# Performance work log

Measured on AMD Instinct MI355X. Metric: run time of the kernel, lower is better.

## Reference

```python
import jax, jax.numpy as jnp
import numpy as np

N_NODES = 50000
N_EDGES = 1250000
D_IN = 64
D_HID = 64
D_OUT = 16
N_GRAPHS = 128


def setup_inputs() -> dict:
    key = jax.random.key(0)
    ks = jax.random.split(key, 16)
    glorot = lambda k, shape: jax.random.normal(k, shape, jnp.float32) * (2.0 / (shape[0] + shape[1])) ** 0.5
    inp = {
        "x": jax.random.normal(ks[0], (N_NODES, D_IN), jnp.float32),
        "edge_index": jax.random.randint(ks[1], (2, N_EDGES), 0, N_NODES, jnp.int32),
        "adj": jnp.zeros((1,), jnp.float32),
        "batch": jnp.sort(jax.random.randint(ks[2], (N_NODES,), 0, N_GRAPHS, jnp.int32)),
        # GraphConv layer 1: lin_rel (with bias) on aggregated msgs, lin_root (no bias) on x
        "W_rel1": glorot(ks[3], (D_IN, D_HID)),
        "b_rel1": jnp.zeros((D_HID,), jnp.float32),
        "W_root1": glorot(ks[4], (D_IN, D_HID)),
        "W_rel2": glorot(ks[5], (D_HID, D_HID)),
        "b_rel2": jnp.zeros((D_HID,), jnp.float32),
        "W_root2": glorot(ks[6], (D_HID, D_HID)),
        "W_rel3": glorot(ks[7], (D_HID, D_HID)),
        "b_rel3": jnp.zeros((D_HID,), jnp.float32),
        "W_root3": glorot(ks[8], (D_HID, D_HID)),
        "W_lin": glorot(ks[9], (D_HID, D_OUT)),
        "b_lin": jnp.zeros((D_OUT,), jnp.float32),
    }
    return inp


def graph_conv(x, src, dst, W_rel, b_rel, W_root):
    # PyG GraphConv (aggr='add'): out[i] = (sum_{j->i} x[j]) @ W_rel + b_rel + x[i] @ W_root
    agg = jax.ops.segment_sum(x[src], dst, num_segments=N_NODES)  # [N, d]
    return agg @ W_rel + b_rel + x @ W_root


def reference(x, edge_index, adj, batch,
              W_rel1, b_rel1, W_root1,
              W_rel2, b_rel2, W_root2,
              W_rel3, b_rel3, W_root3,
              W_lin, b_lin):
    src, dst = edge_index[0], edge_index[1]
    h = jax.nn.relu(graph_conv(x, src, dst, W_rel1, b_rel1, W_root1))
    h = jax.nn.relu(graph_conv(h, src, dst, W_rel2, b_rel2, W_root2))
    h = graph_conv(h, src, dst, W_rel3, b_rel3, W_root3)
    # global_mean_pool over batch ids
    sums = jax.ops.segment_sum(h, batch, num_segments=N_GRAPHS)  # [G, d]
    counts = jax.ops.segment_sum(jnp.ones((h.shape[0],), h.dtype), batch, num_segments=N_GRAPHS)
    pooled = sums / jnp.maximum(counts, 1.0)[:, None]
    return pooled @ W_lin + b_lin  # [G, D_OUT]
```

## Files before the change

### kernel.cpp

```cpp
#include <hip/hip_runtime.h>

#define D 64
#define N_GRAPHS 128
#define D_OUT 16
#define BCAP 16384
#define TILE 4096

typedef unsigned short u16;
typedef unsigned int u32;
typedef unsigned char u8;
typedef __attribute__((ext_vector_type(8))) short bf16x8;
typedef __attribute__((ext_vector_type(4))) float f32x4;

__device__ inline u16 f2bf(float f) {
  u32 u = __float_as_uint(f);
  return (u16)((u + 0x7fffu + ((u >> 16) & 1u)) >> 16);
}
__device__ inline float bf2f(u16 b) { return __uint_as_float((u32)b << 16); }

__global__ __launch_bounds__(256) void cvt_bf16_kernel(
    const float* __restrict__ in, u16* __restrict__ out, int n4,
    int* __restrict__ cursors, int nbuck,
    const float* __restrict__ Wrel1, const float* __restrict__ Wroot1,
    const float* __restrict__ Wrel2, const float* __restrict__ Wroot2,
    const float* __restrict__ Wrel3, const float* __restrict__ Wroot3,
    const float* __restrict__ Wlin, const float* __restrict__ brel3,
    const float* __restrict__ blin,
    float* __restrict__ M1, float* __restrict__ M2, float* __restrict__ cvec,
    u16* __restrict__ WbT1r, u16* __restrict__ WbT1o,
    u16* __restrict__ WbT2r, u16* __restrict__ WbT2o) {
  int t = threadIdx.x;
  if (blockIdx.x == 0) {
    if (t < nbuck) cursors[t] = t * BCAP;
    if (t >= 240) {
      int o = t - 240;
      float c = blin[o];
#pragma unroll
      for (int j = 0; j < D; j++) c = fmaf(brel3[j], Wlin[j * D_OUT + o], c);
      cvec[o] = c;
    }
  } else if (blockIdx.x <= 8) {
    int idx = (blockIdx.x - 1) * 256 + t;
    const float* W = (idx < 1024) ? Wrel3 : Wroot3;
    float* M = (idx < 1024) ? M1 : M2;
    int id = idx & 1023;
    int k = id >> 4, o = id & 15;
    float acc = 0.0f;
#pragma unroll
    for (int j = 0; j < D; j++) acc = fmaf(W[k * D + j], Wlin[j * D_OUT + o], acc);
    M[id] = acc;
  } else if (blockIdx.x <= 16) {
    int tid = (blockIdx.x - 9) * 256 + t;
    int mat = tid >> 9;
    int r = tid & 511;
    int o = r >> 3;
    int k0 = (r & 7) * 8;
    const float* Wsrc = (mat == 0) ? Wrel1 : (mat == 1) ? Wroot1
                       : (mat == 2) ? Wrel2 : Wroot2;
    u16* Wdst = (mat == 0) ? WbT1r : (mat == 1) ? WbT1o
               : (mat == 2) ? WbT2r : WbT2o;
    u16 tmp[8];
#pragma unroll
    for (int j = 0; j < 8; j++) tmp[j] = f2bf(Wsrc[(k0 + j) * D + o]);
    uint4 pw;
    pw.x = (u32)tmp[0] | ((u32)tmp[1] << 16);
    pw.y = (u32)tmp[2] | ((u32)tmp[3] << 16);
    pw.z = (u32)tmp[4] | ((u32)tmp[5] << 16);
    pw.w = (u32)tmp[6] | ((u32)tmp[7] << 16);
    *(uint4*)&Wdst[o * D + k0] = pw;
  }
  int i = blockIdx.x * 256 + t;
  if (i >= n4) return;
  float4 v = ((const float4*)in)[i];
  ushort4 o4;
  o4.x = f2bf(v.x); o4.y = f2bf(v.y); o4.z = f2bf(v.z); o4.w = f2bf(v.w);
  ((ushort4*)out)[i] = o4;
}

__global__ __launch_bounds__(256) void bin_kernel(
    const int* __restrict__ src, const int* __restrict__ dst,
    int* __restrict__ cursors, u32* __restrict__ binned,
    int n_edges, int nbuck) {
  __shared__ u32 ent[TILE];
  __shared__ u8 ebk[TILE];
  __shared__ int hist[256];
  __shared__ int startb[256];
  __shared__ int cur[256];
  __shared__ int gbase[256];
  int t = threadIdx.x;
  hist[t] = 0;
  __syncthreads();

  int base = blockIdx.x * TILE;
  int cnt = n_edges - base;
  if (cnt > TILE) cnt = TILE;

  int mys[16], myd[16];
#pragma unroll
  for (int j = 0; j < 16; j++) {
    int i = base + t + j * 256;
    if (t + j * 256 < cnt) {
      mys[j] = src[i];
      myd[j] = dst[i];
      atomicAdd(&hist[myd[j] >> 8], 1);
    } else {
      myd[j] = -1;
    }
  }
  __syncthreads();
  int myc = hist[t];
  for (int off = 1; off < 256; off <<= 1) {
    int tmp = (t >= off) ? hist[t - off] : 0;
    __syncthreads();
    hist[t] += tmp;
    __syncthreads();
  }
  int excl = hist[t] - myc;
  startb[t] = excl;
  cur[t] = excl;
  __syncthreads();

#pragma unroll
  for (int j = 0; j < 16; j++) {
    if (myd[j] >= 0) {
      int b = myd[j] >> 8;
      int p = atomicAdd(&cur[b], 1);
      ent[p] = ((u32)myd[j] << 16) | (u32)mys[j];
      ebk[p] = (u8)b;
    }
  }
  __syncthreads();

  if (t < nbuck && myc > 0) gbase[t] = atomicAdd(&cursors[t], myc);
  __syncthreads();

#pragma unroll
  for (int j = 0; j < 16; j++) {
    int p = t + j * 256;
    if (p < cnt) {
      int b = ebk[p];
      int gpos = gbase[b] + (p - startb[b]);
      if (gpos < (b + 1) * BCAP) binned[gpos] = ent[p];
    }
  }
}

__global__ __launch_bounds__(256) void csr_kernel(
    const u32* __restrict__ binned, const int* __restrict__ cursors,
    u16* __restrict__ csr_src, int* __restrict__ offsets,
    int n_nodes, int nbuck) {
  __shared__ int deg[256];
  __shared__ int cur[256];
  __shared__ int red[256];
  __shared__ u16 lcsr[BCAP];
  int b = blockIdx.x, t = threadIdx.x;
  int cnt = cursors[b] - b * BCAP;
  if (cnt < 0) cnt = 0;
  if (cnt > BCAP) cnt = BCAP;

  int c = 0;
  if (t < b) {
    c = cursors[t] - t * BCAP;
    if (c < 0) c = 0;
    if (c > BCAP) c = BCAP;
  }
  red[t] = c;
  __syncthreads();
  for (int off = 128; off > 0; off >>= 1) {
    if (t < off) red[t] += red[t + off];
    __syncthreads();
  }
  int ebase = red[0];

  int nodeBase = b << 8;
  int nn = n_nodes - nodeBase;
  if (nn > 256) nn = 256;

  deg[t] = 0;
  __syncthreads();
  const u32* be = binned + (size_t)b * BCAP;
  for (int i = t; i < cnt; i += 256)
    atomicAdd(&deg[(be[i] >> 16) - nodeBase], 1);
  __syncthreads();
  int myd = deg[t];
  for (int off = 1; off < 256; off <<= 1) {
    int tmp = (t >= off) ? deg[t - off] : 0;
    __syncthreads();
    deg[t] += tmp;
    __syncthreads();
  }
  int loff = deg[t] - myd;
  cur[t] = loff;
  if (t < nn) offsets[nodeBase + t] = ebase + loff;
  if (b == nbuck - 1 && t == 0) offsets[n_nodes] = ebase + cnt;
  __syncthreads();

  for (int i = t; i < cnt; i += 256) {
    u32 e = be[i];
    int ln = (e >> 16) - nodeBase;
    int p = atomicAdd(&cur[ln], 1);
    lcsr[p] = (u16)(e & 0xffffu);
  }
  __syncthreads();
  for (int i = t; i < cnt; i += 256) csr_src[ebase + i] = lcsr[i];
}

#define ACC8(a, r)                                                       \
  a[0] += __uint_as_float(r.x << 16); a[1] += __uint_as_float(r.x & 0xffff0000u); \
  a[2] += __uint_as_float(r.y << 16); a[3] += __uint_as_float(r.y & 0xffff0000u); \
  a[4] += __uint_as_float(r.z << 16); a[5] += __uint_as_float(r.z & 0xffff0000u); \
  a[6] += __uint_as_float(r.w << 16); a[7] += __uint_as_float(r.w & 0xffff0000u);

__global__ __launch_bounds__(256) void fused_layer_kernel(
    const u16* __restrict__ h, const int* __restrict__ offsets,
    const u16* __restrict__ csr_src,
    const u16* __restrict__ WbTrel, const u16* __restrict__ WbTroot,
    const float* __restrict__ brel,
    u16* __restrict__ h_out, int n_nodes, int do_relu) {
  __shared__ __align__(16) u16 ldsA[32 * 72];
  __shared__ __align__(16) u16 ldsX[32 * 72];
  int w = threadIdx.x >> 6;
  int lane = threadIdx.x & 63;
  int sub = lane >> 3;
  int fo = (lane & 7) * 8;
  int blockBase = blockIdx.x * 32;
  int nid = blockBase + w * 8 + sub;
  bool valid = nid < n_nodes;
  int node = valid ? nid : 0;
  int start = offsets[node];
  int end = offsets[node + 1];
  if (!valid) end = start;
  int lrow = (w * 8 + sub) * 72;

  uint4 xr = make_uint4(0, 0, 0, 0);
  if (valid) xr = *(const uint4*)(h + ((size_t)node << 6) + fo);
  *(uint4*)&ldsX[lrow + fo] = xr;

  float a0[8] = {0, 0, 0, 0, 0, 0, 0, 0};
  float a1[8] = {0, 0, 0, 0, 0, 0, 0, 0};
  int i = start;
  for (; i + 3 < end; i += 4) {
    int s0 = csr_src[i], s1 = csr_src[i + 1], s2 = csr_src[i + 2], s3 = csr_src[i + 3];
    uint4 r0 = *(const uint4*)(h + ((size_t)s0 << 6) + fo);
    uint4 r1 = *(const uint4*)(h + ((size_t)s1 << 6) + fo);
    uint4 r2 = *(const uint4*)(h + ((size_t)s2 << 6) + fo);
    uint4 r3 = *(const uint4*)(h + ((size_t)s3 << 6) + fo);
    ACC8(a0, r0) ACC8(a1, r1) ACC8(a0, r2) ACC8(a1, r3)
  }
  for (; i < end; i++) {
    int s0 = csr_src[i];
    uint4 r0 = *(const uint4*)(h + ((size_t)s0 << 6) + fo);
    ACC8(a0, r0)
  }
#pragma unroll
  for (int k = 0; k < 8; k++) a0[k] += a1[k];

  uint4 pa;
  pa.x = (u32)f2bf(a0[0]) | ((u32)f2bf(a0[1]) << 16);
  pa.y = (u32)f2bf(a0[2]) | ((u32)f2bf(a0[3]) << 16);
  pa.z = (u32)f2bf(a0[4]) | ((u32)f2bf(a0[5]) << 16);
  pa.w = (u32)f2bf(a0[6]) | ((u32)f2bf(a0[7]) << 16);
  *(uint4*)&ldsA[lrow + fo] = pa;
  __syncthreads();

  int mt = w & 1;
  int ntb = (w >> 1) * 2;
  int lr = lane & 15, lk = lane >> 4;
  int arow = (mt * 16 + lr) * 72;
  bf16x8 af0 = *(const bf16x8*)&ldsA[arow + lk * 8];
  bf16x8 af1 = *(const bf16x8*)&ldsA[arow + 32 + lk * 8];
  bf16x8 xf0 = *(const bf16x8*)&ldsX[arow + lk * 8];
  bf16x8 xf1 = *(const bf16x8*)&ldsX[arow + 32 + lk * 8];
#pragma unroll
  for (int tt = 0; tt < 2; tt++) {
    int nt = ntb + tt;
    int wrow = (nt * 16 + lr) * D + lk * 8;
    bf16x8 br0 = *(const bf16x8*)(WbTrel + wrow);
    bf16x8 br1 = *(const bf16x8*)(WbTrel + wrow + 32);
    bf16x8 bo0 = *(const bf16x8*)(WbTroot + wrow);
    bf16x8 bo1 = *(const bf16x8*)(WbTroot + wrow + 32);
    f32x4 acc = {0.0f, 0.0f, 0.0f, 0.0f};
    acc = __builtin_amdgcn_mfma_f32_16x16x32_bf16(af0, br0, acc, 0, 0, 0);
    acc = __builtin_amdgcn_mfma_f32_16x16x32_bf16(af1, br1, acc, 0, 0, 0);
    acc = __builtin_amdgcn_mfma_f32_16x16x32_bf16(xf0, bo0, acc, 0, 0, 0);
    acc = __builtin_amdgcn_mfma_f32_16x16x32_bf16(xf1, bo1, acc, 0, 0, 0);
    float bias = brel[nt * 16 + lr];
#pragma unroll
    for (int r = 0; r < 4; r++) {
      int onode = blockBase + mt * 16 + lk * 4 + r;
      if (onode < n_nodes) {
        float v = acc[r] + bias;
        if (do_relu) v = fmaxf(v, 0.0f);
        h_out[((size_t)onode << 6) + nt * 16 + lr] = f2bf(v);
      }
    }
  }
}

__global__ __launch_bounds__(256) void gather_kernel(
    const u16* __restrict__ h, const int* __restrict__ offsets,
    const u16* __restrict__ csr_src, float* __restrict__ agg, int n_nodes) {
  int wave = blockIdx.x * 4 + (threadIdx.x >> 6);
  int lane = threadIdx.x & 63;
  int sub = lane >> 3;
  int fo = (lane & 7) * 8;
  int nid = wave * 8 + sub;
  bool valid = nid < n_nodes;
  int node = valid ? nid : 0;
  int start = offsets[node];
  int end = offsets[node + 1];
  if (!valid) end = start;

  float a0[8] = {0, 0, 0, 0, 0, 0, 0, 0};
  float a1[8] = {0, 0, 0, 0, 0, 0, 0, 0};
  int i = start;
  for (; i + 3 < end; i += 4) {
    int s0 = csr_src[i], s1 = csr_src[i + 1], s2 = csr_src[i + 2], s3 = csr_src[i + 3];
    uint4 r0 = *(const uint4*)(h + ((size_t)s0 << 6) + fo);
    uint4 r1 = *(const uint4*)(h + ((size_t)s1 << 6) + fo);
    uint4 r2 = *(const uint4*)(h + ((size_t)s2 << 6) + fo);
    uint4 r3 = *(const uint4*)(h + ((size_t)s3 << 6) + fo);
    ACC8(a0, r0) ACC8(a1, r1) ACC8(a0, r2) ACC8(a1, r3)
  }
  for (; i < end; i++) {
    int s0 = csr_src[i];
    uint4 r0 = *(const uint4*)(h + ((size_t)s0 << 6) + fo);
    ACC8(a0, r0)
  }
#pragma unroll
  for (int k = 0; k < 8; k++) a0[k] += a1[k];
  if (valid) {
    float* ap = agg + ((size_t)node << 6) + fo;
    *(float4*)(ap)     = make_float4(a0[0], a0[1], a0[2], a0[3]);
    *(float4*)(ap + 4) = make_float4(a0[4], a0[5], a0[6], a0[7]);
  }
}

__global__ __launch_bounds__(256) void pool_mean2_kernel(
    const float* __restrict__ aggA, const u16* __restrict__ hH,
    const int* __restrict__ batch, float* __restrict__ pooledA,
    float* __restrict__ pooledH, float* __restrict__ pooledCnt, int n_nodes) {
  __shared__ int seg[2];
  __shared__ float redA[256], redH[256];
  int g = blockIdx.x;
  if (threadIdx.x < 2) {
    int target = g + (int)threadIdx.x;
    int lo = 0, hi = n_nodes;
    while (lo < hi) {
      int mid = (lo + hi) >> 1;
      if (batch[mid] < target) lo = mid + 1; else hi = mid;
    }
    seg[threadIdx.x] = lo;
  }
  __syncthreads();
  int start = seg[0], end = seg[1];
  int f = threadIdx.x & 63, sub = threadIdx.x >> 6;
  float aA = 0.0f, aH = 0.0f;
  for (int n = start + sub; n < end; n += 4) {
    aA += aggA[((size_t)n << 6) + f];
    aH += bf2f(hH[((size_t)n << 6) + f]);
  }
  redA[threadIdx.x] = aA;
  redH[threadIdx.x] = aH;
  __syncthreads();
  if (sub == 0) {
    float vA = redA[f] + redA[64 + f] + redA[128 + f] + redA[192 + f];
    float vH = redH[f] + redH[64 + f] + redH[128 + f] + redH[192 + f];
    float cnt = (float)(end - start);
    float inv = 1.0f / fmaxf(cnt, 1.0f);
    pooledA[g * D + f] = vA * inv;
    pooledH[g * D + f] = vH * inv;
    if (f == 0) pooledCnt[g] = cnt;
  }
}

__global__ __launch_bounds__(256) void final2_kernel(
    const float* __restrict__ pooledA, const float* __restrict__ pooledH,
    const float* __restrict__ M1, const float* __restrict__ M2,
    const float* __restrict__ cvec, const float* __restrict__ blin,
    const float* __restrict__ pooledCnt, float* __restrict__ out) {
  int idx = blockIdx.x * 256 + threadIdx.x;
  if (idx >= N_GRAPHS * D_OUT) return;
  int g = idx >> 4;
  int o = idx & 15;
  float acc = (pooledCnt[g] > 0.0f) ? cvec[o] : blin[o];
#pragma unroll
  for (int k = 0; k < D; k++) {
    acc = fmaf(pooledA[g * D + k], M1[k * D_OUT + o], acc);
    acc = fmaf(pooledH[g * D + k], M2[k * D_OUT + o], acc);
  }
  out[idx] = acc;
}

extern "C" void kernel_launch(void* const* d_in, const int* in_sizes, int n_in,
                              void* d_out, int out_size, void* d_ws, size_t ws_size,
                              hipStream_t stream) {
  const float* x     = (const float*)d_in[0];
  const int*   ei    = (const int*)d_in[1];
  const int*   batch = (const int*)d_in[3];
  const float* Wrel1 = (const float*)d_in[4];
  const float* brel1 = (const float*)d_in[5];
  const float* Wroot1= (const float*)d_in[6];
  const float* Wrel2 = (const float*)d_in[7];
  const float* brel2 = (const float*)d_in[8];
  const float* Wroot2= (const float*)d_in[9];
  const float* Wrel3 = (const float*)d_in[10];
  const float* brel3 = (const float*)d_in[11];
  const float* Wroot3= (const float*)d_in[12];
  const float* Wlin  = (const float*)d_in[13];
  const float* blin  = (const float*)d_in[14];
  float* out = (float*)d_out;

  const int n_edges = in_sizes[1] / 2;
  const int n_nodes = in_sizes[0] / D;
  const int* src = ei;
  const int* dst = ei + n_edges;
  const int nbuck = (n_nodes + 255) >> 8;

  char* p = (char*)d_ws;
  size_t binned_bytes = (size_t)nbuck * BCAP * sizeof(u32);
  size_t agg_bytes = (size_t)n_nodes * D * sizeof(float);
  u32* binned  = (u32*)p;
  float* agg   = (float*)p;
  p += (binned_bytes > agg_bytes ? binned_bytes : agg_bytes);
  float* pooledA = (float*)p; p += (size_t)N_GRAPHS * D * sizeof(float);
  float* pooledH = (float*)p; p += (size_t)N_GRAPHS * D * sizeof(float);
  float* pooledCnt = (float*)p; p += (size_t)N_GRAPHS * sizeof(float);
  float* M1     = (float*)p; p += (size_t)D * D_OUT * sizeof(float);
  float* M2     = (float*)p; p += (size_t)D * D_OUT * sizeof(float);
  float* cvec   = (float*)p; p += 16 * sizeof(float);
  int* cursors  = (int*)p;   p += 256 * sizeof(int);
  int* offsets  = (int*)p;   p += (size_t)(n_nodes + 4) * sizeof(int);
  u16* hX       = (u16*)p;   p += (size_t)n_nodes * D * sizeof(u16);
  u16* h1       = (u16*)p;   p += (size_t)n_nodes * D * sizeof(u16);
  u16* h2       = (u16*)p;   p += (size_t)n_nodes * D * sizeof(u16);
  u16* csr_src  = (u16*)p;   p += (size_t)n_edges * sizeof(u16);
  u16* WbT1r    = (u16*)p;   p += (size_t)D * D * sizeof(u16);
  u16* WbT1o    = (u16*)p;   p += (size_t)D * D * sizeof(u16);
  u16* WbT2r    = (u16*)p;   p += (size_t)D * D * sizeof(u16);
  u16* WbT2o    = (u16*)p;   p += (size_t)D * D * sizeof(u16);

  const int bin_blocks = (n_edges + TILE - 1) / TILE;
  const int fused_blocks = (n_nodes + 31) / 32;
  const int gath_blocks = (n_nodes + 31) / 32;
  const int cvt_n4 = n_nodes * D / 4;

  cvt_bf16_kernel<<<(cvt_n4 + 255) / 256, 256, 0, stream>>>(
      x, hX, cvt_n4, cursors, nbuck, Wrel1, Wroot1, Wrel2, Wroot2,
      Wrel3, Wroot3, Wlin, brel3, blin, M1, M2, cvec,
      WbT1r, WbT1o, WbT2r, WbT2o);
  bin_kernel<<<bin_blocks, 256, 0, stream>>>(src, dst, cursors, binned, n_edges, nbuck);
  csr_kernel<<<nbuck, 256, 0, stream>>>(binned, cursors, csr_src, offsets, n_nodes, nbuck);

  fused_layer_kernel<<<fused_blocks, 256, 0, stream>>>(
      hX, offsets, csr_src, WbT1r, WbT1o, brel1, h1, n_nodes, 1);
  fused_layer_kernel<<<fused_blocks, 256, 0, stream>>>(
      h1, offsets, csr_src, WbT2r, WbT2o, brel2, h2, n_nodes, 1);

  gather_kernel<<<gath_blocks, 256, 0, stream>>>(h2, offsets, csr_src, agg, n_nodes);

  pool_mean2_kernel<<<N_GRAPHS, 256, 0, stream>>>(agg, h2, batch, pooledA, pooledH, pooledCnt, n_nodes);
  final2_kernel<<<(N_GRAPHS * D_OUT + 255) / 256, 256, 0, stream>>>(
      pooledA, pooledH, M1, M2, cvec, blin, pooledCnt, out);
}
```

Baseline: 256.2 us.

## Degree-sort nodes per wave, pack bf16 accumulation, fuse pool and final kernels

Each 32-node block now ranks its nodes by in-degree in a shared-memory prologue and assigns them to 8-lane groups in sorted order, so each wave holds nodes of similar degree and wastes fewer idle lanes in the gather loop. The accumulators become two-float vectors to allow packed adds. The pooling kernel and the final projection kernel are merged into one launch, which drops the intermediate pooled buffers. The prologue costs two extra barriers and an O(32) rank loop per block.

```diff
diff --git a/kernel.cpp b/kernel.cpp
--- a/kernel.cpp
+++ b/kernel.cpp
@@ -11,12 +11,16 @@
 typedef unsigned char u8;
 typedef __attribute__((ext_vector_type(8))) short bf16x8;
 typedef __attribute__((ext_vector_type(4))) float f32x4;
+typedef __attribute__((ext_vector_type(2))) float f32x2;
 
 __device__ inline u16 f2bf(float f) {
   u32 u = __float_as_uint(f);
   return (u16)((u + 0x7fffu + ((u >> 16) & 1u)) >> 16);
 }
 __device__ inline float bf2f(u16 b) { return __uint_as_float((u32)b << 16); }
+__device__ inline f32x2 bfpair(u32 v) {
+  return (f32x2){__uint_as_float(v << 16), __uint_as_float(v & 0xffff0000u)};
+}
 
 __global__ __launch_bounds__(256) void cvt_bf16_kernel(
     const float* __restrict__ in, u16* __restrict__ out, int n4,
@@ -205,11 +209,29 @@
   for (int i = t; i < cnt; i += 256) csr_src[ebase + i] = lcsr[i];
 }
 
-#define ACC8(a, r)                                                       \
-  a[0] += __uint_as_float(r.x << 16); a[1] += __uint_as_float(r.x & 0xffff0000u); \
-  a[2] += __uint_as_float(r.y << 16); a[3] += __uint_as_float(r.y & 0xffff0000u); \
-  a[4] += __uint_as_float(r.z << 16); a[5] += __uint_as_float(r.z & 0xffff0000u); \
-  a[6] += __uint_as_float(r.w << 16); a[7] += __uint_as_float(r.w & 0xffff0000u);
+#define ACC8(a, r) \
+  a[0] += bfpair(r.x); a[1] += bfpair(r.y); a[2] += bfpair(r.z); a[3] += bfpair(r.w);
+
+#define BALANCE_PROLOGUE(soff, permAr, blockBase, n_nodes, offsets)     \
+  {                                                                     \
+    int t_ = threadIdx.x;                                               \
+    if (t_ < 33) {                                                      \
+      int idx = blockBase + t_;                                         \
+      if (idx > n_nodes) idx = n_nodes;                                 \
+      soff[t_] = offsets[idx];                                          \
+    }                                                                   \
+    __syncthreads();                                                    \
+    if (t_ < 32) {                                                      \
+      int d_ = (blockBase + t_ < n_nodes) ? soff[t_ + 1] - soff[t_] : -1; \
+      int r_ = 0;                                                       \
+      for (int j_ = 0; j_ < 32; j_++) {                                 \
+        int dj_ = (blockBase + j_ < n_nodes) ? soff[j_ + 1] - soff[j_] : -1; \
+        if (dj_ > d_ || (dj_ == d_ && j_ < t_)) r_++;                   \
+      }                                                                 \
+      permAr[r_] = (u8)t_;                                              \
+    }                                                                   \
+    __syncthreads();                                                    \
+  }
 
 __global__ __launch_bounds__(256) void fused_layer_kernel(
     const u16* __restrict__ h, const int* __restrict__ offsets,
@@ -219,25 +241,30 @@
     u16* __restrict__ h_out, int n_nodes, int do_relu) {
   __shared__ __align__(16) u16 ldsA[32 * 72];
   __shared__ __align__(16) u16 ldsX[32 * 72];
+  __shared__ int soff[33];
+  __shared__ u8 permAr[32];
   int w = threadIdx.x >> 6;
   int lane = threadIdx.x & 63;
   int sub = lane >> 3;
   int fo = (lane & 7) * 8;
   int blockBase = blockIdx.x * 32;
-  int nid = blockBase + w * 8 + sub;
-  bool valid = nid < n_nodes;
-  int node = valid ? nid : 0;
-  int start = offsets[node];
-  int end = offsets[node + 1];
+
+  BALANCE_PROLOGUE(soff, permAr, blockBase, n_nodes, offsets)
+
+  int ln = permAr[w * 8 + sub];
+  int node = blockBase + ln;
+  bool valid = node < n_nodes;
+  int start = soff[ln];
+  int end = soff[ln + 1];
   if (!valid) end = start;
-  int lrow = (w * 8 + sub) * 72;
+  int lrow = ln * 72;
 
   uint4 xr = make_uint4(0, 0, 0, 0);
   if (valid) xr = *(const uint4*)(h + ((size_t)node << 6) + fo);
   *(uint4*)&ldsX[lrow + fo] = xr;
 
-  float a0[8] = {0, 0, 0, 0, 0, 0, 0, 0};
-  float a1[8] = {0, 0, 0, 0, 0, 0, 0, 0};
+  f32x2 a0[4] = {{0,0},{0,0},{0,0},{0,0}};
+  f32x2 a1[4] = {{0,0},{0,0},{0,0},{0,0}};
   int i = start;
   for (; i + 3 < end; i += 4) {
     int s0 = csr_src[i], s1 = csr_src[i + 1], s2 = csr_src[i + 2], s3 = csr_src[i + 3];
@@ -253,13 +280,13 @@
     ACC8(a0, r0)
   }
 #pragma unroll
-  for (int k = 0; k < 8; k++) a0[k] += a1[k];
+  for (int k = 0; k < 4; k++) a0[k] += a1[k];
 
   uint4 pa;
-  pa.x = (u32)f2bf(a0[0]) | ((u32)f2bf(a0[1]) << 16);
-  pa.y = (u32)f2bf(a0[2]) | ((u32)f2bf(a0[3]) << 16);
-  pa.z = (u32)f2bf(a0[4]) | ((u32)f2bf(a0[5]) << 16);
-  pa.w = (u32)f2bf(a0[6]) | ((u32)f2bf(a0[7]) << 16);
+  pa.x = (u32)f2bf(a0[0].x) | ((u32)f2bf(a0[0].y) << 16);
+  pa.y = (u32)f2bf(a0[1].x) | ((u32)f2bf(a0[1].y) << 16);
+  pa.z = (u32)f2bf(a0[2].x) | ((u32)f2bf(a0[2].y) << 16);
+  pa.w = (u32)f2bf(a0[3].x) | ((u32)f2bf(a0[3].y) << 16);
   *(uint4*)&ldsA[lrow + fo] = pa;
   __syncthreads();
 
@@ -300,19 +327,25 @@
 __global__ __launch_bounds__(256) void gather_kernel(
     const u16* __restrict__ h, const int* __restrict__ offsets,
     const u16* __restrict__ csr_src, float* __restrict__ agg, int n_nodes) {
-  int wave = blockIdx.x * 4 + (threadIdx.x >> 6);
+  __shared__ int soff[33];
+  __shared__ u8 permAr[32];
+  int w = threadIdx.x >> 6;
   int lane = threadIdx.x & 63;
   int sub = lane >> 3;
   int fo = (lane & 7) * 8;
-  int nid = wave * 8 + sub;
-  bool valid = nid < n_nodes;
-  int node = valid ? nid : 0;
-  int start = offsets[node];
-  int end = offsets[node + 1];
+  int blockBase = blockIdx.x * 32;
+
+  BALANCE_PROLOGUE(soff, permAr, blockBase, n_nodes, offsets)
+
+  int ln = permAr[w * 8 + sub];
+  int node = blockBase + ln;
+  bool valid = node < n_nodes;
+  int start = soff[ln];
+  int end = soff[ln + 1];
   if (!valid) end = start;
 
-  float a0[8] = {0, 0, 0, 0, 0, 0, 0, 0};
-  float a1[8] = {0, 0, 0, 0, 0, 0, 0, 0};
+  f32x2 a0[4] = {{0,0},{0,0},{0,0},{0,0}};
+  f32x2 a1[4] = {{0,0},{0,0},{0,0},{0,0}};
   int i = start;
   for (; i + 3 < end; i += 4) {
     int s0 = csr_src[i], s1 = csr_src[i + 1], s2 = csr_src[i + 2], s3 = csr_src[i + 3];
@@ -328,68 +361,63 @@
     ACC8(a0, r0)
   }
 #pragma unroll
-  for (int k = 0; k < 8; k++) a0[k] += a1[k];
+  for (int k = 0; k < 4; k++) a0[k] += a1[k];
   if (valid) {
     float* ap = agg + ((size_t)node << 6) + fo;
-    *(float4*)(ap)     = make_float4(a0[0], a0[1], a0[2], a0[3]);
-    *(float4*)(ap + 4) = make_float4(a0[4], a0[5], a0[6], a0[7]);
-  }
-}
-
-__global__ __launch_bounds__(256) void pool_mean2_kernel(
+    *(float4*)(ap)     = make_float4(a0[0].x, a0[0].y, a0[1].x, a0[1].y);
+    *(float4*)(ap + 4) = make_float4(a0[2].x, a0[2].y, a0[3].x, a0[3].y);
+  }
+}
+
+__global__ __launch_bounds__(256) void pool_final_kernel(
     const float* __restrict__ aggA, const u16* __restrict__ hH,
-    const int* __restrict__ batch, float* __restrict__ pooledA,
-    float* __restrict__ pooledH, float* __restrict__ pooledCnt, int n_nodes) {
+    const int* __restrict__ batch,
+    const float* __restrict__ M1, const float* __restrict__ M2,
+    const float* __restrict__ cvec, const float* __restrict__ blin,
+    float* __restrict__ out, int n_nodes) {
   __shared__ int seg[2];
   __shared__ float redA[256], redH[256];
+  __shared__ float mA[64], mH[64];
   int g = blockIdx.x;
-  if (threadIdx.x < 2) {
-    int target = g + (int)threadIdx.x;
+  int t = threadIdx.x;
+  if (t < 2) {
+    int target = g + t;
     int lo = 0, hi = n_nodes;
     while (lo < hi) {
       int mid = (lo + hi) >> 1;
       if (batch[mid] < target) lo = mid + 1; else hi = mid;
     }
-    seg[threadIdx.x] = lo;
+    seg[t] = lo;
   }
   __syncthreads();
   int start = seg[0], end = seg[1];
-  int f = threadIdx.x & 63, sub = threadIdx.x >> 6;
+  int f = t & 63, sub = t >> 6;
   float aA = 0.0f, aH = 0.0f;
   for (int n = start + sub; n < end; n += 4) {
     aA += aggA[((size_t)n << 6) + f];
     aH += bf2f(hH[((size_t)n << 6) + f]);
   }
-  redA[threadIdx.x] = aA;
-  redH[threadIdx.x] = aH;
+  redA[t] = aA;
+  redH[t] = aH;
   __syncthreads();
   if (sub == 0) {
-    float vA = redA[f] + redA[64 + f] + redA[128 + f] + redA[192 + f];
-    float vH = redH[f] + redH[64 + f] + redH[128 + f] + redH[192 + f];
-    float cnt = (float)(end - start);
-    float inv = 1.0f / fmaxf(cnt, 1.0f);
-    pooledA[g * D + f] = vA * inv;
-    pooledH[g * D + f] = vH * inv;
-    if (f == 0) pooledCnt[g] = cnt;
-  }
-}
-
-__global__ __launch_bounds__(256) void final2_kernel(
-    const float* __restrict__ pooledA, const float* __restrict__ pooledH,
-    const float* __restrict__ M1, const float* __restrict__ M2,
-    const float* __restrict__ cvec, const float* __restrict__ blin,
-    const float* __restrict__ pooledCnt, float* __restrict__ out) {
-  int idx = blockIdx.x * 256 + threadIdx.x;
-  if (idx >= N_GRAPHS * D_OUT) return;
-  int g = idx >> 4;
-  int o = idx & 15;
-  float acc = (pooledCnt[g] > 0.0f) ? cvec[o] : blin[o];
-#pragma unroll
-  for (int k = 0; k < D; k++) {
-    acc = fmaf(pooledA[g * D + k], M1[k * D_OUT + o], acc);
-    acc = fmaf(pooledH[g * D + k], M2[k * D_OUT + o], acc);
-  }
-  out[idx] = acc;
+    float inv = (end > start) ? 1.0f / (float)(end - start) : 0.0f;
+    mA[f] = (redA[f] + redA[64 + f] + redA[128 + f] + redA[192 + f]) * inv;
+    mH[f] = (redH[f] + redH[64 + f] + redH[128 + f] + redH[192 + f]) * inv;
+  }
+  __syncthreads();
+  if (t < 16) {
+    float acc;
+    if (end > start) {
+      acc = cvec[t];
+#pragma unroll
+      for (int k = 0; k < D; k++)
+        acc = fmaf(mA[k], M1[k * D_OUT + t], fmaf(mH[k], M2[k * D_OUT + t], acc));
+    } else {
+      acc = blin[t];
+    }
+    out[g * D_OUT + t] = acc;
+  }
 }
 
 extern "C" void kernel_launch(void* const* d_in, const int* in_sizes, int n_in,
@@ -423,9 +451,6 @@
   u32* binned  = (u32*)p;
   float* agg   = (float*)p;
   p += (binned_bytes > agg_bytes ? binned_bytes : agg_bytes);
-  float* pooledA = (float*)p; p += (size_t)N_GRAPHS * D * sizeof(float);
-  float* pooledH = (float*)p; p += (size_t)N_GRAPHS * D * sizeof(float);
-  float* pooledCnt = (float*)p; p += (size_t)N_GRAPHS * sizeof(float);
   float* M1     = (float*)p; p += (size_t)D * D_OUT * sizeof(float);
   float* M2     = (float*)p; p += (size_t)D * D_OUT * sizeof(float);
   float* cvec   = (float*)p; p += 16 * sizeof(float);
@@ -442,7 +467,6 @@
 
   const int bin_blocks = (n_edges + TILE - 1) / TILE;
   const int fused_blocks = (n_nodes + 31) / 32;
-  const int gath_blocks = (n_nodes + 31) / 32;
   const int cvt_n4 = n_nodes * D / 4;
 
   cvt_bf16_kernel<<<(cvt_n4 + 255) / 256, 256, 0, stream>>>(
@@ -457,9 +481,8 @@
   fused_layer_kernel<<<fused_blocks, 256, 0, stream>>>(
       h1, offsets, csr_src, WbT2r, WbT2o, brel2, h2, n_nodes, 1);
 
-  gather_kernel<<<gath_blocks, 256, 0, stream>>>(h2, offsets, csr_src, agg, n_nodes);
-
-  pool_mean2_kernel<<<N_GRAPHS, 256, 0, stream>>>(agg, h2, batch, pooledA, pooledH, pooledCnt, n_nodes);
-  final2_kernel<<<(N_GRAPHS * D_OUT + 255) / 256, 256, 0, stream>>>(
-      pooledA, pooledH, M1, M2, cvec, blin, pooledCnt, out);
-}
+  gather_kernel<<<fused_blocks, 256, 0, stream>>>(h2, offsets, csr_src, agg, n_nodes);
+
+  pool_final_kernel<<<N_GRAPHS, 256, 0, stream>>>(
+      agg, h2, batch, M1, M2, cvec, blin, out, n_nodes);
+}
```

After: 257.7 us. About the same (+0.6%).
